# Kernel tuning notes

Hardware: AMD Instinct MI355X
Metric: run time of the kernel (lower is better)

The kernel has to match this reference:

```python
import jax, jax.numpy as jnp
import numpy as np

EMBED = 1024
HEADS = 16
HEAD_DIM = EMBED // HEADS
NEG = -1e20


def setup_inputs() -> dict:
    key = jax.random.key(0)
    ks = jax.random.split(key, 12)
    N, S, E = 2, 2048, EMBED
    w = lambda k: (jax.random.normal(k, (E, E), dtype=jnp.float32) * 0.02)
    b = lambda k: (jax.random.normal(k, (E,), dtype=jnp.float32) * 0.02)
    return {
        "values": jax.random.normal(ks[0], (N, S, E), dtype=jnp.float32),
        "keys": jax.random.normal(ks[1], (N, S, E), dtype=jnp.float32),
        "query": jax.random.normal(ks[2], (N, S, E), dtype=jnp.float32),
        "mask": jnp.ones((N, S), dtype=jnp.int32),
        "Wv": w(ks[3]), "bv": b(ks[4]),
        "Wk": w(ks[5]), "bk": b(ks[6]),
        "Wq": w(ks[7]), "bq": b(ks[8]),
        "Wo": w(ks[9]), "bo": b(ks[10]),
    }


def reference(values, keys, query, mask, Wv, bv, Wk, bk, Wq, bq, Wo, bo):
    N, S, E = query.shape
    # torch nn.Linear: x @ W.T + b
    v = (values @ Wv.T + bv).reshape(N, S, HEADS, HEAD_DIM)
    k = (keys @ Wk.T + bk).reshape(N, S, HEADS, HEAD_DIM)
    q = (query @ Wq.T + bq).reshape(N, S, HEADS, HEAD_DIM)
    # full [N,H,Q,K] score matrix, as in the original einsum
    energy = jnp.einsum('nqhd,nkhd->nhqk', q, k)
    # 2D mask with mismatched dims triggers causal tril path in the original
    causal = jnp.tril(jnp.ones((S, S), dtype=bool))  # [Q,K]
    energy = jnp.where(causal[None, None, :, :], energy, NEG)
    # NOTE: original scales by sqrt(embed_size), not sqrt(head_dim)
    attn = jax.nn.softmax(energy / jnp.sqrt(jnp.float32(E)), axis=3)
    out = jnp.einsum('nhqk,nkhd->nqhd', attn, v).reshape(N, S, E)
    return out @ Wo.T + bo
```

## Files before the change

kernel.cpp:

```cpp
#include <hip/hip_runtime.h>

typedef __bf16 bf16;
typedef __bf16 bf16x4 __attribute__((ext_vector_type(4)));
typedef __bf16 bf16x8 __attribute__((ext_vector_type(8)));
typedef float floatx4 __attribute__((ext_vector_type(4)));

#define GLOAD_LDS16(gp, lp) \
  __builtin_amdgcn_global_load_lds( \
      (const __attribute__((address_space(1))) void*)(gp), \
      (__attribute__((address_space(3))) void*)(lp), 16, 0, 0)

__global__ __launch_bounds__(256) void cvt_all_kernel(
    const float* __restrict__ v, const float* __restrict__ k, const float* __restrict__ q,
    const float* __restrict__ wv, const float* __restrict__ wk,
    const float* __restrict__ wq, const float* __restrict__ wo,
    bf16* __restrict__ xv, bf16* __restrict__ xk, bf16* __restrict__ xq,
    bf16* __restrict__ bwv, bf16* __restrict__ bwk, bf16* __restrict__ bwq,
    bf16* __restrict__ bwo) {
  const int i = blockIdx.x * 256 + threadIdx.x;
  const int A4 = 1 << 20;
  const float* src; bf16* dst; int off;
  if (i < A4)            { src = v; dst = xv; off = i; }
  else if (i < 2 * A4)   { src = k; dst = xk; off = i - A4; }
  else if (i < 3 * A4)   { src = q; dst = xq; off = i - 2 * A4; }
  else {
    int j = i - 3 * A4; int r = j >> 18; off = j & ((1 << 18) - 1);
    src = (r == 0) ? wv : (r == 1) ? wk : (r == 2) ? wq : wo;
    dst = (r == 0) ? bwv : (r == 1) ? bwk : (r == 2) ? bwq : bwo;
  }
  float4 x = reinterpret_cast<const float4*>(src)[off];
  union { bf16 b[4]; short4 s; } u;
  u.b[0] = (bf16)x.x; u.b[1] = (bf16)x.y; u.b[2] = (bf16)x.z; u.b[3] = (bf16)x.w;
  reinterpret_cast<short4*>(dst)[off] = u.s;
}

template <int MODE>
__device__ __forceinline__ void gemm_body(
    const bf16* __restrict__ A, const bf16* __restrict__ B,
    const float* __restrict__ bias, void* __restrict__ Cout) {
  constexpr int K = 1024, N = 1024;
  __shared__ __align__(16) bf16 SMEM[8192];
  bf16* As = SMEM;
  bf16* Bs = SMEM + 4096;
  const int tid = threadIdx.x;
  const int lane = tid & 63;
  const int wave = tid >> 6;
  const int quad = lane >> 4;
  const int l16 = lane & 15;
  const int wm = (wave >> 1) * 64;
  const int wn = (wave & 1) * 64;
  const int am0 = blockIdx.y * 128;
  const int bn0 = blockIdx.x * 128;
  const int srow = lane >> 2;
  const int scol = (lane & 3) * 8;

  floatx4 acc[4][4] = {};

  for (int k0 = 0; k0 < K; k0 += 32) {
    __syncthreads();
#pragma unroll
    for (int j = 0; j < 2; j++) {
      const int chunk = wave * 2 + j;
      const int row = chunk * 16 + srow;
      GLOAD_LDS16(A + (size_t)(am0 + row) * K + k0 + scol, As + chunk * 512);
      GLOAD_LDS16(B + (size_t)(bn0 + row) * K + k0 + scol, Bs + chunk * 512);
    }
    __syncthreads();

    bf16x8 af[4], bfv[4];
#pragma unroll
    for (int mi = 0; mi < 4; mi++)
      af[mi] = *reinterpret_cast<const bf16x8*>(&As[(wm + mi * 16 + l16) * 32 + quad * 8]);
#pragma unroll
    for (int ni = 0; ni < 4; ni++)
      bfv[ni] = *reinterpret_cast<const bf16x8*>(&Bs[(wn + ni * 16 + l16) * 32 + quad * 8]);
#pragma unroll
    for (int mi = 0; mi < 4; mi++)
#pragma unroll
      for (int ni = 0; ni < 4; ni++)
        acc[mi][ni] = __builtin_amdgcn_mfma_f32_16x16x32_bf16(af[mi], bfv[ni], acc[mi][ni], 0, 0, 0);
  }

  if constexpr (MODE == 2) {
#pragma unroll
    for (int mi = 0; mi < 4; mi++) {
#pragma unroll
      for (int ni = 0; ni < 4; ni++) {
        const int col = bn0 + wn + ni * 16 + l16;
        const float bb = bias[col];
        const int row = am0 + wm + mi * 16 + quad * 4;
#pragma unroll
        for (int r = 0; r < 4; r++)
          reinterpret_cast<float*>(Cout)[(size_t)(row + r) * N + col] = acc[mi][ni][r] + bb;
      }
    }
  } else {
    __syncthreads();
    bf16* T = SMEM + wave * 2048;
    const int nb = (am0 + wm) >> 11;
    const int sq0 = (am0 + wm) & 2047;
    const int h = (bn0 + wn) >> 6;
    const int nh = nb * 16 + h;
    const int r8 = lane >> 3, c8 = lane & 7;

    if constexpr (MODE == 0) {
#pragma unroll
      for (int pp = 0; pp < 2; pp++) {
#pragma unroll
        for (int mm = 0; mm < 2; mm++) {
          const int mi = pp * 2 + mm;
#pragma unroll
          for (int ni = 0; ni < 4; ni++) {
            const int d = ni * 16 + l16;
            const float bc = bias[bn0 + wn + d];
#pragma unroll
            for (int r = 0; r < 4; r++) {
              const int s = mm * 16 + quad * 4 + r;
              T[s * 64 + (d & 7) + 8 * ((d >> 3) ^ (s & 7))] = (bf16)(acc[mi][ni][r] + bc);
            }
          }
        }
#pragma unroll
        for (int it = 0; it < 4; it++) {
          const int s = it * 8 + r8;
          bf16x8 vv = *reinterpret_cast<const bf16x8*>(&T[s * 64 + ((c8 ^ r8) * 8)]);
          *reinterpret_cast<bf16x8*>(
              reinterpret_cast<bf16*>(Cout) +
              ((size_t)nh * 2048 + sq0 + pp * 32 + s) * 64 + c8 * 8) = vv;
        }
      }
    } else {
#pragma unroll
      for (int pp = 0; pp < 2; pp++) {
#pragma unroll
        for (int nn = 0; nn < 2; nn++) {
          const int ni = pp * 2 + nn;
          const int dp = nn * 16 + l16;
          const float bc = bias[bn0 + wn + pp * 32 + dp];
#pragma unroll
          for (int mi = 0; mi < 4; mi++) {
#pragma unroll
            for (int r = 0; r < 4; r++) {
              const int s = mi * 16 + quad * 4 + r;
              T[dp * 64 + (s & 7) + 8 * ((s >> 3) ^ (dp & 7))] = (bf16)(acc[mi][ni][r] + bc);
            }
          }
        }
#pragma unroll
        for (int it = 0; it < 4; it++) {
          const int dp = it * 8 + r8;
          bf16x8 vv = *reinterpret_cast<const bf16x8*>(&T[dp * 64 + ((c8 ^ r8) * 8)]);
          *reinterpret_cast<bf16x8*>(
              reinterpret_cast<bf16*>(Cout) +
              ((size_t)nh * 64 + pp * 32 + dp) * 2048 + sq0 + c8 * 8) = vv;
        }
      }
    }
  }
}

__global__ __launch_bounds__(256) void gemm_qkv(
    const bf16* __restrict__ A0, const bf16* __restrict__ B0, const float* __restrict__ c0, bf16* __restrict__ C0,
    const bf16* __restrict__ A1, const bf16* __restrict__ B1, const float* __restrict__ c1, bf16* __restrict__ C1,
    const bf16* __restrict__ A2, const bf16* __restrict__ B2, const float* __restrict__ c2, bf16* __restrict__ C2) {
  if (blockIdx.z == 0)      gemm_body<0>(A0, B0, c0, C0);
  else if (blockIdx.z == 1) gemm_body<0>(A1, B1, c1, C1);
  else                      gemm_body<1>(A2, B2, c2, C2);
}

__global__ __launch_bounds__(256) void gemm_out(
    const bf16* __restrict__ A, const bf16* __restrict__ B,
    const float* __restrict__ bias, float* __restrict__ C) {
  gemm_body<2>(A, B, bias, C);
}

#define S_LEN 2048
#define EMB 1024
#define QT 128
#define KTILE 64
#define PSTR 72
#define SCALE2 (0.03125f * 1.44269504f)

__global__ __launch_bounds__(256) void attn_kernel(
    const bf16* __restrict__ Qh, const bf16* __restrict__ Kh,
    const bf16* __restrict__ Vt, bf16* __restrict__ O,
    float* __restrict__ Opart, float* __restrict__ lpart) {
  __shared__ __align__(16) bf16 Ks[KTILE * 64];
  __shared__ __align__(16) bf16 Vs[64 * KTILE];
  __shared__ __align__(16) bf16 Ps[QT * PSTR];

  const int tid = threadIdx.x;
  const int lane = tid & 63;
  const int wave = tid >> 6;
  const int quad = lane >> 4;
  const int l16 = lane & 15;
  const int wq = wave * 32;

  const int c = blockIdx.x;
  const int role = blockIdx.y;
  const int nh = c >> 3;
  const int t = c & 7;
  const int n = nh >> 4;
  const int h = nh & 15;
  int qt, kt0, kt1;
  if (role == 0) { qt = t; kt0 = 0; kt1 = 2 * t + 2; }
  else {
    qt = 15 - t;
    const int halfk = qt + 1;
    kt0 = (role == 1) ? 0 : halfk;
    kt1 = (role == 1) ? halfk : 2 * halfk;
  }
  const int q0 = qt * QT;

  bf16x8 aq[2][2];
  {
    const bf16* Qb = Qh + ((size_t)nh * S_LEN + q0 + wq + l16) * 64 + quad * 8;
#pragma unroll
    for (int mi = 0; mi < 2; mi++)
#pragma unroll
      for (int kc = 0; kc < 2; kc++)
        aq[mi][kc] = *reinterpret_cast<const bf16x8*>(Qb + mi * 16 * 64 + kc * 32);
  }

  float l_part[2][4] = {};
  floatx4 o_acc[2][4] = {};

  const bf16* Kbase = Kh + (size_t)nh * S_LEN * 64;
  const bf16* Vbase = Vt + (size_t)nh * 64 * S_LEN;

  const int srl = lane >> 3;
  const int sc8 = lane & 7;

  for (int kt = kt0; kt < kt1; kt++) {
    const int k0 = kt * KTILE;

    __syncthreads();
#pragma unroll
    for (int j = 0; j < 2; j++) {
      const int rl = wave * 16 + j * 8 + srl;
      const int c8s = ((sc8 ^ (rl & 7)) * 8);
      GLOAD_LDS16(Kbase + (size_t)(k0 + rl) * 64 + c8s, Ks + (wave * 16 + j * 8) * 64);
      GLOAD_LDS16(Vbase + (size_t)rl * S_LEN + k0 + c8s, Vs + (wave * 16 + j * 8) * 64);
    }
    __syncthreads();

    floatx4 s_acc[2][4] = {};
#pragma unroll
    for (int kc = 0; kc < 2; kc++) {
      bf16x8 bk[4];
#pragma unroll
      for (int ni = 0; ni < 4; ni++)
        bk[ni] = *reinterpret_cast<const bf16x8*>(
            &Ks[(ni * 16 + l16) * 64 + (((kc * 4 + quad) ^ (l16 & 7)) * 8)]);
#pragma unroll
      for (int mi = 0; mi < 2; mi++)
#pragma unroll
        for (int ni = 0; ni < 4; ni++)
          s_acc[mi][ni] = __builtin_amdgcn_mfma_f32_16x16x32_bf16(aq[mi][kc], bk[ni], s_acc[mi][ni], 0, 0, 0);
    }

    const bool needMask = (k0 + KTILE - 1) > (q0 + wq);
#pragma unroll
    for (int mi = 0; mi < 2; mi++) {
#pragma unroll
      for (int ni = 0; ni < 4; ni++) {
        const int cg = k0 + ni * 16 + l16;
#pragma unroll
        for (int r = 0; r < 4; r++) {
          const int rg = q0 + wq + mi * 16 + quad * 4 + r;
          float pr = __builtin_amdgcn_exp2f(s_acc[mi][ni][r] * SCALE2);
          if (needMask) pr = (cg <= rg) ? pr : 0.f;
          s_acc[mi][ni][r] = pr;
          l_part[mi][r] += pr;
        }
      }
    }

#pragma unroll
    for (int mi = 0; mi < 2; mi++) {
#pragma unroll
      for (int ni = 0; ni < 4; ni++) {
        const int cl = ni * 2 + (l16 >> 3);
        const int pc = (cl ^ quad) * 8 + (l16 & 7);
#pragma unroll
        for (int r = 0; r < 4; r++)
          Ps[(wq + mi * 16 + quad * 4 + r) * PSTR + pc] = (bf16)s_acc[mi][ni][r];
      }
    }

#pragma unroll
    for (int kc = 0; kc < 2; kc++) {
      bf16x8 ap[2], bv[4];
      const int pc = ((kc * 4 + quad) ^ (l16 >> 2)) * 8;
#pragma unroll
      for (int mi = 0; mi < 2; mi++)
        ap[mi] = *reinterpret_cast<const bf16x8*>(&Ps[(wq + mi * 16 + l16) * PSTR + pc]);
#pragma unroll
      for (int di = 0; di < 4; di++)
        bv[di] = *reinterpret_cast<const bf16x8*>(
            &Vs[(di * 16 + l16) * 64 + (((kc * 4 + quad) ^ (l16 & 7)) * 8)]);
#pragma unroll
      for (int mi = 0; mi < 2; mi++)
#pragma unroll
        for (int di = 0; di < 4; di++)
          o_acc[mi][di] = __builtin_amdgcn_mfma_f32_16x16x32_bf16(ap[mi], bv[di], o_acc[mi][di], 0, 0, 0);
    }
  }

#pragma unroll
  for (int mi = 0; mi < 2; mi++)
#pragma unroll
    for (int r = 0; r < 4; r++) {
      float s = l_part[mi][r];
#pragma unroll
      for (int off = 1; off < 16; off <<= 1) s += __shfl_xor(s, off);
      l_part[mi][r] = s;
    }

  if (role == 0) {
    bf16* Op = O + ((size_t)(n * S_LEN + q0 + wq)) * EMB + h * 64;
#pragma unroll
    for (int mi = 0; mi < 2; mi++) {
#pragma unroll
      for (int r = 0; r < 4; r++) {
        const float inv = 1.0f / l_part[mi][r];
        bf16* orow = Op + (size_t)(mi * 16 + quad * 4 + r) * EMB;
#pragma unroll
        for (int di = 0; di < 4; di++)
          orow[di * 16 + l16] = (bf16)(o_acc[mi][di][r] * inv);
      }
    }
  } else {
    float* Ob = Opart + ((size_t)c * 2 + (role - 1)) * (QT * 64);
    float* lb = lpart + ((size_t)c * 2 + (role - 1)) * QT;
#pragma unroll
    for (int mi = 0; mi < 2; mi++)
#pragma unroll
      for (int r = 0; r < 4; r++)
        if (l16 == 0) lb[wq + mi * 16 + quad * 4 + r] = l_part[mi][r];
#pragma unroll
    for (int mi = 0; mi < 2; mi++)
#pragma unroll
      for (int r = 0; r < 4; r++) {
        float* orow = Ob + (size_t)(wq + mi * 16 + quad * 4 + r) * 64;
#pragma unroll
        for (int di = 0; di < 4; di++)
          orow[di * 16 + l16] = o_acc[mi][di][r];
      }
  }
}

__global__ __launch_bounds__(256) void attn_combine(
    const float* __restrict__ Opart, const float* __restrict__ lpart,
    bf16* __restrict__ O) {
  const int c = blockIdx.x;
  const int nh = c >> 3;
  const int t = c & 7;
  const int qt = 15 - t;
  const int n = nh >> 4;
  const int h = nh & 15;
  const float* O1 = Opart + (size_t)c * 2 * (QT * 64);
  const float* O2 = O1 + QT * 64;
  const float* l1 = lpart + (size_t)c * 2 * QT;
  const float* l2 = l1 + QT;
  const int tid = threadIdx.x;
  for (int i = tid; i < QT * 64 / 4; i += 256) {
    const int row = i >> 4;
    const float inv = 1.0f / (l1[row] + l2[row]);
    float4 a = reinterpret_cast<const float4*>(O1)[i];
    float4 b = reinterpret_cast<const float4*>(O2)[i];
    bf16x4 pk;
    pk[0] = (bf16)((a.x + b.x) * inv);
    pk[1] = (bf16)((a.y + b.y) * inv);
    pk[2] = (bf16)((a.z + b.z) * inv);
    pk[3] = (bf16)((a.w + b.w) * inv);
    *reinterpret_cast<bf16x4*>(
        O + ((size_t)(n * S_LEN + qt * QT + row)) * EMB + h * 64 + (i & 15) * 4) = pk;
  }
}

extern "C" void kernel_launch(void* const* d_in, const int* in_sizes, int n_in,
                              void* d_out, int out_size, void* d_ws, size_t ws_size,
                              hipStream_t stream) {
  (void)in_sizes; (void)n_in; (void)out_size; (void)ws_size;
  const float* values = (const float*)d_in[0];
  const float* keys   = (const float*)d_in[1];
  const float* query  = (const float*)d_in[2];
  const float* Wv = (const float*)d_in[4];
  const float* bv = (const float*)d_in[5];
  const float* Wk = (const float*)d_in[6];
  const float* bk = (const float*)d_in[7];
  const float* Wq = (const float*)d_in[8];
  const float* bq = (const float*)d_in[9];
  const float* Wo = (const float*)d_in[10];
  const float* bo = (const float*)d_in[11];
  float* out = (float*)d_out;

  const int NB = 2, S = 2048, E = 1024;
  const int M = NB * S;
  const size_t MB_ = 1u << 20;
  char* ws = (char*)d_ws;
  bf16* xv  = (bf16*)(ws + 0 * MB_);
  bf16* xk  = (bf16*)(ws + 8 * MB_);
  bf16* xq  = (bf16*)(ws + 16 * MB_);
  bf16* wvb = (bf16*)(ws + 24 * MB_);
  bf16* wkb = (bf16*)(ws + 26 * MB_);
  bf16* wqb = (bf16*)(ws + 28 * MB_);
  bf16* wob = (bf16*)(ws + 30 * MB_);
  bf16* kh  = (bf16*)(ws + 32 * MB_);
  bf16* qh  = (bf16*)(ws + 40 * MB_);
  bf16* vt  = (bf16*)(ws + 48 * MB_);
  bf16* ao  = (bf16*)(ws + 56 * MB_);
  float* Opart = (float*)(ws + 0 * MB_);
  float* lpart = (float*)(ws + 17 * MB_);

  cvt_all_kernel<<<(4 << 20) / 256, 256, 0, stream>>>(
      values, keys, query, Wv, Wk, Wq, Wo,
      xv, xk, xq, wvb, wkb, wqb, wob);

  gemm_qkv<<<dim3(E / 128, M / 128, 3), 256, 0, stream>>>(
      xq, wqb, bq, qh,
      xk, wkb, bk, kh,
      xv, wvb, bv, vt);

  attn_kernel<<<dim3(256, 3), 256, 0, stream>>>(qh, kh, vt, ao, Opart, lpart);
  attn_combine<<<dim3(256), 256, 0, stream>>>(Opart, lpart, ao);

  gemm_out<<<dim3(E / 128, M / 128), 256, 0, stream>>>(ao, wob, bo, out);
}
```

Measured before the change: 242.5 us.

## Double-buffer K/V tiles and transpose the QK MFMA so P is written as packed vectors

K and V tiles now go into two LDS buffers, and the next tile is prefetched through global_load_lds while the current one is computed, leaving one barrier per iteration. The QK^T MFMA operands are swapped, so each lane holds four consecutive key columns for a single query row. This lets P be written to LDS as packed bf16x4 vectors instead of scalar swizzled stores, and the row-sum reduction shrinks to two cross-quad shuffles. The cost is double the K/V LDS footprint, which may lower occupancy, and the P layout is no longer swizzled, so some LDS bank conflicts may appear.

After: 234.3 us. 3.4% less time.

```diff
diff --git a/kernel.cpp b/kernel.cpp
--- a/kernel.cpp
+++ b/kernel.cpp
@@ -185,8 +185,8 @@
     const bf16* __restrict__ Qh, const bf16* __restrict__ Kh,
     const bf16* __restrict__ Vt, bf16* __restrict__ O,
     float* __restrict__ Opart, float* __restrict__ lpart) {
-  __shared__ __align__(16) bf16 Ks[KTILE * 64];
-  __shared__ __align__(16) bf16 Vs[64 * KTILE];
+  __shared__ __align__(16) bf16 Ks[2 * KTILE * 64];
+  __shared__ __align__(16) bf16 Vs[2 * 64 * KTILE];
   __shared__ __align__(16) bf16 Ps[QT * PSTR];
 
   const int tid = threadIdx.x;
@@ -222,7 +222,7 @@
         aq[mi][kc] = *reinterpret_cast<const bf16x8*>(Qb + mi * 16 * 64 + kc * 32);
   }
 
-  float l_part[2][4] = {};
+  float l_part[2] = {};
   floatx4 o_acc[2][4] = {};
 
   const bf16* Kbase = Kh + (size_t)nh * S_LEN * 64;
@@ -231,18 +231,25 @@
   const int srl = lane >> 3;
   const int sc8 = lane & 7;
 
-  for (int kt = kt0; kt < kt1; kt++) {
-    const int k0 = kt * KTILE;
-
-    __syncthreads();
+  auto stage = [&](int kt) {
+    const int k0s = kt * KTILE;
+    const int buf = (kt & 1) * 4096;
 #pragma unroll
     for (int j = 0; j < 2; j++) {
       const int rl = wave * 16 + j * 8 + srl;
       const int c8s = ((sc8 ^ (rl & 7)) * 8);
-      GLOAD_LDS16(Kbase + (size_t)(k0 + rl) * 64 + c8s, Ks + (wave * 16 + j * 8) * 64);
-      GLOAD_LDS16(Vbase + (size_t)rl * S_LEN + k0 + c8s, Vs + (wave * 16 + j * 8) * 64);
-    }
+      GLOAD_LDS16(Kbase + (size_t)(k0s + rl) * 64 + c8s, Ks + buf + (wave * 16 + j * 8) * 64);
+      GLOAD_LDS16(Vbase + (size_t)rl * S_LEN + k0s + c8s, Vs + buf + (wave * 16 + j * 8) * 64);
+    }
+  };
+
+  stage(kt0);
+  for (int kt = kt0; kt < kt1; kt++) {
+    const int k0 = kt * KTILE;
     __syncthreads();
+    if (kt + 1 < kt1) stage(kt + 1);
+    const bf16* Kc = Ks + (kt & 1) * 4096;
+    const bf16* Vc = Vs + (kt & 1) * 4096;
 
     floatx4 s_acc[2][4] = {};
 #pragma unroll
@@ -251,54 +258,45 @@
 #pragma unroll
       for (int ni = 0; ni < 4; ni++)
         bk[ni] = *reinterpret_cast<const bf16x8*>(
-            &Ks[(ni * 16 + l16) * 64 + (((kc * 4 + quad) ^ (l16 & 7)) * 8)]);
+            &Kc[(ni * 16 + l16) * 64 + (((kc * 4 + quad) ^ (l16 & 7)) * 8)]);
 #pragma unroll
       for (int mi = 0; mi < 2; mi++)
 #pragma unroll
         for (int ni = 0; ni < 4; ni++)
-          s_acc[mi][ni] = __builtin_amdgcn_mfma_f32_16x16x32_bf16(aq[mi][kc], bk[ni], s_acc[mi][ni], 0, 0, 0);
+          s_acc[mi][ni] = __builtin_amdgcn_mfma_f32_16x16x32_bf16(bk[ni], aq[mi][kc], s_acc[mi][ni], 0, 0, 0);
     }
 
     const bool needMask = (k0 + KTILE - 1) > (q0 + wq);
+    const int qg = q0 + wq + l16;
 #pragma unroll
     for (int mi = 0; mi < 2; mi++) {
 #pragma unroll
       for (int ni = 0; ni < 4; ni++) {
-        const int cg = k0 + ni * 16 + l16;
+        const int kgb = k0 + ni * 16 + quad * 4;
+        bf16x4 pk;
 #pragma unroll
         for (int r = 0; r < 4; r++) {
-          const int rg = q0 + wq + mi * 16 + quad * 4 + r;
           float pr = __builtin_amdgcn_exp2f(s_acc[mi][ni][r] * SCALE2);
-          if (needMask) pr = (cg <= rg) ? pr : 0.f;
-          s_acc[mi][ni][r] = pr;
-          l_part[mi][r] += pr;
+          if (needMask) pr = ((kgb + r) <= (qg + mi * 16)) ? pr : 0.f;
+          l_part[mi] += pr;
+          pk[r] = (bf16)pr;
         }
-      }
-    }
-
-#pragma unroll
-    for (int mi = 0; mi < 2; mi++) {
-#pragma unroll
-      for (int ni = 0; ni < 4; ni++) {
-        const int cl = ni * 2 + (l16 >> 3);
-        const int pc = (cl ^ quad) * 8 + (l16 & 7);
-#pragma unroll
-        for (int r = 0; r < 4; r++)
-          Ps[(wq + mi * 16 + quad * 4 + r) * PSTR + pc] = (bf16)s_acc[mi][ni][r];
+        *reinterpret_cast<bf16x4*>(
+            &Ps[(wq + mi * 16 + l16) * PSTR + ni * 16 + quad * 4]) = pk;
       }
     }
 
 #pragma unroll
     for (int kc = 0; kc < 2; kc++) {
       bf16x8 ap[2], bv[4];
-      const int pc = ((kc * 4 + quad) ^ (l16 >> 2)) * 8;
 #pragma unroll
       for (int mi = 0; mi < 2; mi++)
-        ap[mi] = *reinterpret_cast<const bf16x8*>(&Ps[(wq + mi * 16 + l16) * PSTR + pc]);
+        ap[mi] = *reinterpret_cast<const bf16x8*>(
+            &Ps[(wq + mi * 16 + l16) * PSTR + kc * 32 + quad * 8]);
 #pragma unroll
       for (int di = 0; di < 4; di++)
         bv[di] = *reinterpret_cast<const bf16x8*>(
-            &Vs[(di * 16 + l16) * 64 + (((kc * 4 + quad) ^ (l16 & 7)) * 8)]);
+            &Vc[(di * 16 + l16) * 64 + (((kc * 4 + quad) ^ (l16 & 7)) * 8)]);
 #pragma unroll
       for (int mi = 0; mi < 2; mi++)
 #pragma unroll
@@ -307,23 +305,23 @@
     }
   }
 
-#pragma unroll
-  for (int mi = 0; mi < 2; mi++)
-#pragma unroll
-    for (int r = 0; r < 4; r++) {
-      float s = l_part[mi][r];
-#pragma unroll
-      for (int off = 1; off < 16; off <<= 1) s += __shfl_xor(s, off);
-      l_part[mi][r] = s;
-    }
+  float l_sum[2];
+#pragma unroll
+  for (int mi = 0; mi < 2; mi++) {
+    float s = l_part[mi];
+    s += __shfl_xor(s, 16);
+    s += __shfl_xor(s, 32);
+    l_sum[mi] = s;
+  }
 
   if (role == 0) {
     bf16* Op = O + ((size_t)(n * S_LEN + q0 + wq)) * EMB + h * 64;
 #pragma unroll
     for (int mi = 0; mi < 2; mi++) {
+      const float linv = 1.0f / l_sum[mi];
 #pragma unroll
       for (int r = 0; r < 4; r++) {
-        const float inv = 1.0f / l_part[mi][r];
+        const float inv = __shfl(linv, quad * 4 + r);
         bf16* orow = Op + (size_t)(mi * 16 + quad * 4 + r) * EMB;
 #pragma unroll
         for (int di = 0; di < 4; di++)
@@ -335,9 +333,7 @@
     float* lb = lpart + ((size_t)c * 2 + (role - 1)) * QT;
 #pragma unroll
     for (int mi = 0; mi < 2; mi++)
-#pragma unroll
-      for (int r = 0; r < 4; r++)
-        if (l16 == 0) lb[wq + mi * 16 + quad * 4 + r] = l_part[mi][r];
+      if (lane < 16) lb[wq + mi * 16 + lane] = l_sum[mi];
 #pragma unroll
     for (int mi = 0; mi < 2; mi++)
 #pragma unroll
```
